# Performance work log

Measured on AMD Instinct MI355X. Metric: run time of the kernel, lower is better.

Reference implementation:

```python
import jax, jax.numpy as jnp
import numpy as np

B, S, D = 4, 512, 768
NH, DH = 12, 64
EXP_N, INV_N = 32, 64


def _scalar_mlp(x, w1, b1, w2, b2):
    # elementwise 1 -> N -> 1 MLP: y = relu(x*w1 + b1) @ w2 + b2, applied per element
    h = jax.nn.relu(x[..., None] * w1 + b1)          # [..., N]
    return jnp.einsum('...n,n->...', h, w2) + b2[0]  # [...]


def fit_softmax(X, exp_w1, exp_b1, exp_w2, exp_b2, inv_w1, inv_b1, inv_w2, inv_b2):
    # X: [B, H, S, S]. Faithful to torch fit_softmax: reference value is X[:, :, 0]
    tmax = X[:, :, 0][..., None]                      # [B, H, S, 1]
    tp = jnp.minimum(X - (tmax - 1.0), 3.0)           # clamp tp > 3 -> 3
    exp_val = _scalar_mlp(tp, exp_w1, exp_b1, exp_w2, exp_b2)
    X_up = jnp.where(tp > -20.0, exp_val, 0.0)        # only index tp > -20
    partition = jnp.sum(X_up, axis=-1, keepdims=True)  # [B, H, S, 1]
    p_inv = _scalar_mlp(partition, inv_w1, inv_b1, inv_w2, inv_b2)
    out = X_up * p_inv
    partition_p2 = jnp.sum(out, axis=-1, keepdims=True)
    p_inv2 = _scalar_mlp(partition_p2, inv_w1, inv_b1, inv_w2, inv_b2)
    # renormalize only rows whose partition exceeds 1.5
    return jnp.where(partition_p2 > 1.5, out * p_inv2, out)


def setup_inputs() -> dict:
    key = jax.random.key(0)
    ks = jax.random.split(key, 16)
    f = jax.random.normal
    return {
        'hidden_states': f(ks[0], (B, S, D), jnp.float32),
        'attention_mask': jnp.zeros((B, 1, 1, S), jnp.float32),
        'Wq': f(ks[1], (D, D), jnp.float32) * 0.02,
        'bq': f(ks[2], (D,), jnp.float32) * 0.02,
        'Wk': f(ks[3], (D, D), jnp.float32) * 0.02,
        'bk': f(ks[4], (D,), jnp.float32) * 0.02,
        'Wv': f(ks[5], (D, D), jnp.float32) * 0.02,
        'bv': f(ks[6], (D,), jnp.float32) * 0.02,
        'exp_w1': f(ks[7], (EXP_N,), jnp.float32),
        'exp_b1': f(ks[8], (EXP_N,), jnp.float32),
        'exp_w2': f(ks[9], (EXP_N,), jnp.float32) * 0.1,
        'exp_b2': f(ks[10], (1,), jnp.float32) * 0.1,
        'inv_w1': f(ks[11], (INV_N,), jnp.float32),
        'inv_b1': f(ks[12], (INV_N,), jnp.float32),
        'inv_w2': f(ks[13], (INV_N,), jnp.float32) * 0.1,
        'inv_b2': f(ks[14], (1,), jnp.float32) * 0.1,
    }


def reference(hidden_states, attention_mask, Wq, bq, Wk, bk, Wv, bv,
              exp_w1, exp_b1, exp_w2, exp_b2, inv_w1, inv_b1, inv_w2, inv_b2):
    def split_heads(x):  # [B, S, D] -> [B, H, S, DH]
        return x.reshape(B, S, NH, DH).transpose(0, 2, 1, 3)

    q = split_heads(hidden_states @ Wq.T + bq)
    k = split_heads(hidden_states @ Wk.T + bk)
    v = split_heads(hidden_states @ Wv.T + bv)

    scores = jnp.einsum('bhqd,bhkd->bhqk', q, k) / np.float32(np.sqrt(DH))
    scores = scores + attention_mask
    probs = fit_softmax(scores, exp_w1, exp_b1, exp_w2, exp_b2,
                        inv_w1, inv_b1, inv_w2, inv_b2)
    ctx = jnp.einsum('bhqk,bhkd->bhqd', probs, v)     # [B, H, S, DH]
    return ctx.transpose(0, 2, 1, 3).reshape(B, S, D)
```

## Files before the change

kernel.cpp:

```cpp
#include <hip/hip_runtime.h>
#include <math.h>

typedef unsigned short u16;
typedef short bf16x8 __attribute__((ext_vector_type(8)));
typedef float f32x4 __attribute__((ext_vector_type(4)));

#define BN 4
#define SN 512
#define DN 768
#define NHN 12
#define DHN 64
#define EXPN 32
#define INVN 64

#define TAB_T0 -20.5f
#define TAB_DLT (23.5f / 512.0f)
#define TAB_SCALE (512.0f / 23.5f)

__device__ __forceinline__ u16 f2b(float f) {
    union { float f; unsigned int u; } v; v.f = f;
    unsigned int r = v.u + 0x7FFFu + ((v.u >> 16) & 1u);
    return (u16)(r >> 16);
}
__device__ __forceinline__ u16 f2h(float f) {
    union { _Float16 h; u16 u; } v; v.h = (_Float16)f; return v.u;
}

#define GLD16(g, l) __builtin_amdgcn_global_load_lds( \
    (__attribute__((address_space(1))) const void*)(g), \
    (__attribute__((address_space(3))) void*)(l), 16, 0, 0)

__global__ __launch_bounds__(256) void prep(
    const float* __restrict__ X, const float* __restrict__ Wq,
    const float* __restrict__ Wk, const float* __restrict__ Wv,
    const float* __restrict__ ew1, const float* __restrict__ eb1,
    const float* __restrict__ ew2, const float* __restrict__ eb2,
    u16* __restrict__ Xb, u16* __restrict__ Wqb,
    u16* __restrict__ Wkb, u16* __restrict__ Wvb,
    float2* __restrict__ tbl)
{
    if (blockIdx.y == 4) {
        int i = blockIdx.x * 256 + threadIdx.x;
        if (i > 513) return;
        float t0 = TAB_T0 + i * TAB_DLT;
        float t1 = t0 + TAB_DLT;
        float y0 = eb2[0], y1 = y0;
        #pragma unroll 8
        for (int n = 0; n < EXPN; ++n) {
            float w1 = ew1[n], b1 = eb1[n], w2 = ew2[n];
            y0 += fmaxf(fmaf(t0, w1, b1), 0.f) * w2;
            y1 += fmaxf(fmaf(t1, w1, b1), 0.f) * w2;
        }
        tbl[i] = make_float2(y0, y1 - y0);
        return;
    }
    const float* s; u16* d; int n;
    switch (blockIdx.y) {
        case 0:  s = X;  d = Xb;  n = (BN * SN) * DN; break;
        case 1:  s = Wq; d = Wqb; n = DN * DN; break;
        case 2:  s = Wk; d = Wkb; n = DN * DN; break;
        default: s = Wv; d = Wvb; n = DN * DN; break;
    }
    int i = (blockIdx.x * 256 + threadIdx.x) * 4;
    if (i < n) {
        float4 v = *(const float4*)&s[i];
        unsigned int lo = (unsigned)f2b(v.x) | ((unsigned)f2b(v.y) << 16);
        unsigned int hi = (unsigned)f2b(v.z) | ((unsigned)f2b(v.w) << 16);
        *(uint2*)&d[i] = make_uint2(lo, hi);
    }
}

__global__ __launch_bounds__(256) void qkv_mfma(
    const u16* __restrict__ Xb,
    const u16* __restrict__ Wqb, const u16* __restrict__ Wkb, const u16* __restrict__ Wvb,
    const float* __restrict__ bq, const float* __restrict__ bk, const float* __restrict__ bv,
    u16* __restrict__ Qb, u16* __restrict__ Kb, u16* __restrict__ Vtr)
{
    __shared__ __align__(16) u16 As[128 * 32];
    __shared__ __align__(16) u16 Bs[64 * 32];

    const int tid = threadIdx.x, w = tid >> 6, l = tid & 63;
    const int lr = l & 15, lg = l >> 4;
    const int m0 = blockIdx.y * 128;
    const int nsel = blockIdx.x / 12;
    const int n0l = (blockIdx.x % 12) * 64;
    const u16* W = (nsel == 0) ? Wqb : (nsel == 1) ? Wkb : Wvb;
    const float* bias = (nsel == 0) ? bq : (nsel == 1) ? bk : bv;
    u16* out = (nsel == 0) ? Qb : (nsel == 1) ? Kb : Vtr;

    const int wm = w >> 1, wn = w & 1;

    const int oA0 = tid * 16;
    const int rA0 = oA0 >> 6, sA0 = (oA0 >> 4) & 3;
    const int cA0 = (sA0 ^ ((rA0 >> 1) & 3)) * 8;
    const int oA1 = oA0 + 4096;
    const int rA1 = oA1 >> 6, sA1 = (oA1 >> 4) & 3;
    const int cA1 = (sA1 ^ ((rA1 >> 1) & 3)) * 8;
    const u16* gA0 = Xb + (m0 + rA0) * DN + cA0;
    const u16* gA1 = Xb + (m0 + rA1) * DN + cA1;
    const u16* gB  = W + (n0l + rA0) * DN + cA0;

    int offA[4], offB[2];
    #pragma unroll
    for (int mi = 0; mi < 4; ++mi) {
        int row = wm * 64 + mi * 16 + lr;
        offA[mi] = row * 64 + ((lg ^ ((row >> 1) & 3)) * 16);
    }
    #pragma unroll
    for (int ni = 0; ni < 2; ++ni) {
        int row = wn * 32 + ni * 16 + lr;
        offB[ni] = row * 64 + ((lg ^ ((row >> 1) & 3)) * 16);
    }

    f32x4 acc[4][2];
    #pragma unroll
    for (int mi = 0; mi < 4; ++mi)
        #pragma unroll
        for (int ni = 0; ni < 2; ++ni) acc[mi][ni] = (f32x4){0.f, 0.f, 0.f, 0.f};

    for (int k0 = 0; k0 < DN; k0 += 32) {
        __syncthreads();
        GLD16(gA0 + k0, (char*)As + oA0);
        GLD16(gA1 + k0, (char*)As + oA1);
        GLD16(gB  + k0, (char*)Bs + oA0);
        __syncthreads();

        bf16x8 af[4], bff[2];
        #pragma unroll
        for (int mi = 0; mi < 4; ++mi) af[mi] = *(const bf16x8*)((const char*)As + offA[mi]);
        #pragma unroll
        for (int ni = 0; ni < 2; ++ni) bff[ni] = *(const bf16x8*)((const char*)Bs + offB[ni]);
        #pragma unroll
        for (int mi = 0; mi < 4; ++mi)
            #pragma unroll
            for (int ni = 0; ni < 2; ++ni)
                acc[mi][ni] = __builtin_amdgcn_mfma_f32_16x16x32_bf16(af[mi], bff[ni], acc[mi][ni], 0, 0, 0);
    }

    if (nsel < 2) {
        #pragma unroll
        for (int ni = 0; ni < 2; ++ni) {
            int col = n0l + wn * 32 + ni * 16 + lr;
            float bc = bias[col];
            int hh = col >> 6, dh = col & 63;
            #pragma unroll
            for (int mi = 0; mi < 4; ++mi) {
                #pragma unroll
                for (int r = 0; r < 4; ++r) {
                    int m = m0 + wm * 64 + mi * 16 + lg * 4 + r;
                    int bi = m >> 9, srow = m & 511;
                    out[(((bi * NHN + hh) * SN) + srow) * DHN + dh] = f2b(acc[mi][ni][r] + bc);
                }
            }
        }
    } else {
        #pragma unroll
        for (int ni = 0; ni < 2; ++ni) {
            int col = n0l + wn * 32 + ni * 16 + lr;
            float bc = bias[col];
            int hh = col >> 6, dh = col & 63;
            #pragma unroll
            for (int mi = 0; mi < 4; ++mi) {
                int m = m0 + wm * 64 + mi * 16 + lg * 4;
                int bi = m >> 9, srow = m & 511;
                ushort4 pk;
                pk.x = f2h(acc[mi][ni][0] + bc);
                pk.y = f2h(acc[mi][ni][1] + bc);
                pk.z = f2h(acc[mi][ni][2] + bc);
                pk.w = f2h(acc[mi][ni][3] + bc);
                *(ushort4*)&out[((size_t)(bi * NHN + hh) * DHN + dh) * SN + srow] = pk;
            }
        }
    }
}

__global__ __launch_bounds__(512, 6) void attn_mfma(
    const u16* __restrict__ Qb, const u16* __restrict__ Kb, const u16* __restrict__ Vtr,
    const float* __restrict__ mask, const float2* __restrict__ tbl,
    const float* __restrict__ iw1, const float* __restrict__ ib1,
    const float* __restrict__ iw2, const float* __restrict__ ib2,
    float* __restrict__ out)
{
    __shared__ __align__(16) u16 sb[32 * 512];
    __shared__ __align__(16) float2 tab[514];
    __shared__ float ms[SN];
    __shared__ float wI1[INVN], wIb1[INVN], wI2[INVN];
    __shared__ float partw[8][32];
    __shared__ float scale_s[32];
    __shared__ float pvbuf[32][68];
    __shared__ float scal;

    const int tid = threadIdx.x, w = tid >> 6, l = tid & 63;
    const int lr = l & 15, lg = l >> 4, kb8 = lg * 8;
    const int bid = blockIdx.x;
    const int bh = bid >> 4;
    const int q0 = (bid & 15) * 32;
    const int b = bh / NHN, h = bh % NHN;
    const u16* Qh = Qb + (size_t)bh * SN * DHN;
    const u16* Kh = Kb + (size_t)bh * SN * DHN;
    const u16* VTh = Vtr + (size_t)bh * DHN * SN;

    if (tid < INVN) { wI1[tid] = iw1[tid]; wIb1[tid] = ib1[tid]; wI2[tid] = iw2[tid]; }
    if (tid == 511) scal = ib2[0];
    if (tid < SN) ms[tid] = mask[b * SN + tid];
    for (int i = tid; i < 514; i += 512) tab[i] = tbl[i];
    __syncthreads();

    const float ib2v = scal;

    bf16x8 aq00 = *(const bf16x8*)(Qh + (q0 + lr) * DHN + kb8);
    bf16x8 aq01 = *(const bf16x8*)(Qh + (q0 + lr) * DHN + 32 + kb8);
    bf16x8 aq10 = *(const bf16x8*)(Qh + (q0 + 16 + lr) * DHN + kb8);
    bf16x8 aq11 = *(const bf16x8*)(Qh + (q0 + 16 + lr) * DHN + 32 + kb8);

    float myref0[4], myref1[4];
    {
        bf16x8 a00 = *(const bf16x8*)(Qh + kb8);
        bf16x8 a01 = *(const bf16x8*)(Qh + 32 + kb8);
        const u16* kp0 = Kh + (q0 + lr) * DHN + kb8;
        bf16x8 b00 = *(const bf16x8*)(kp0);
        bf16x8 b01 = *(const bf16x8*)(kp0 + 32);
        const u16* kp1 = Kh + (q0 + 16 + lr) * DHN + kb8;
        bf16x8 b10 = *(const bf16x8*)(kp1);
        bf16x8 b11 = *(const bf16x8*)(kp1 + 32);
        f32x4 d0 = {0.f, 0.f, 0.f, 0.f}, d1 = {0.f, 0.f, 0.f, 0.f};
        d0 = __builtin_amdgcn_mfma_f32_16x16x32_bf16(a00, b00, d0, 0, 0, 0);
        d0 = __builtin_amdgcn_mfma_f32_16x16x32_bf16(a01, b01, d0, 0, 0, 0);
        d1 = __builtin_amdgcn_mfma_f32_16x16x32_bf16(a00, b10, d1, 0, 0, 0);
        d1 = __builtin_amdgcn_mfma_f32_16x16x32_bf16(a01, b11, d1, 0, 0, 0);
        float rc0 = d0[0] * 0.125f + ms[q0 + lr];
        float rc1 = d1[0] * 0.125f + ms[q0 + 16 + lr];
        #pragma unroll
        for (int r = 0; r < 4; ++r) {
            myref0[r] = __shfl(rc0, lg * 4 + r);
            myref1[r] = __shfl(rc1, lg * 4 + r);
        }
    }

    char* sbb = (char*)sb;
    float part0[4] = {0.f, 0.f, 0.f, 0.f};
    float part1[4] = {0.f, 0.f, 0.f, 0.f};
    const u16* kpp = Kh + (w * 64 + lr) * DHN + kb8;
    bf16x8 nb0 = *(const bf16x8*)(kpp);
    bf16x8 nb1 = *(const bf16x8*)(kpp + 32);
    #pragma unroll
    for (int i = 0; i < 4; ++i) {
        bf16x8 b0 = nb0, b1 = nb1;
        if (i < 3) {
            const u16* kn = kpp + (i + 1) * 16 * DHN;
            nb0 = *(const bf16x8*)(kn);
            nb1 = *(const bf16x8*)(kn + 32);
        }
        f32x4 d0 = {0.f, 0.f, 0.f, 0.f}, d1 = {0.f, 0.f, 0.f, 0.f};
        d0 = __builtin_amdgcn_mfma_f32_16x16x32_bf16(aq00, b0, d0, 0, 0, 0);
        d0 = __builtin_amdgcn_mfma_f32_16x16x32_bf16(aq01, b1, d0, 0, 0, 0);
        d1 = __builtin_amdgcn_mfma_f32_16x16x32_bf16(aq10, b0, d1, 0, 0, 0);
        d1 = __builtin_amdgcn_mfma_f32_16x16x32_bf16(aq11, b1, d1, 0, 0, 0);
        const int col0 = w * 64 + i * 16;
        const float mv = ms[col0 + lr];
        const int colb = (col0 + lr) * 2;
        #pragma unroll
        for (int r = 0; r < 4; ++r) {
            {
                float tp = fminf(d0[r] * 0.125f + mv - (myref0[r] - 1.0f), 3.0f);
                float v = (tp - TAB_T0) * TAB_SCALE;
                int idx = (int)v;
                idx = idx < 0 ? 0 : idx;
                float fr = v - (float)idx;
                float2 p = tab[idx];
                float e = fmaf(fr, p.y, p.x);
                float xu = (tp > -20.0f) ? e : 0.f;
                part0[r] += xu;
                int row = lg * 4 + r;
                *(u16*)(sbb + row * 1024 + (colb ^ ((row & 7) << 4))) = f2h(xu);
            }
            {
                float tp = fminf(d1[r] * 0.125f + mv - (myref1[r] - 1.0f), 3.0f);
                float v = (tp - TAB_T0) * TAB_SCALE;
                int idx = (int)v;
                idx = idx < 0 ? 0 : idx;
                float fr = v - (float)idx;
                float2 p = tab[idx];
                float e = fmaf(fr, p.y, p.x);
                float xu = (tp > -20.0f) ? e : 0.f;
                part1[r] += xu;
                int row = 16 + lg * 4 + r;
                *(u16*)(sbb + row * 1024 + (colb ^ ((row & 7) << 4))) = f2h(xu);
            }
        }
    }
    #pragma unroll
    for (int r = 0; r < 4; ++r) {
        #pragma unroll
        for (int s = 1; s < 16; s <<= 1) {
            part0[r] += __shfl_xor(part0[r], s);
            part1[r] += __shfl_xor(part1[r], s);
        }
    }
    if (lr == 0) {
        #pragma unroll
        for (int r = 0; r < 4; ++r) {
            partw[w][lg * 4 + r] = part0[r];
            partw[w][16 + lg * 4 + r] = part1[r];
        }
    }
    __syncthreads();

    #pragma unroll
    for (int rr = 0; rr < 4; ++rr) {
        const int row = w * 4 + rr;
        float pt = 0.f;
        #pragma unroll
        for (int ww = 0; ww < 8; ++ww) pt += partw[ww][row];
        float hu = fmaxf(fmaf(pt, wI1[l], wIb1[l]), 0.f) * wI2[l];
        #pragma unroll
        for (int s = 32; s > 0; s >>= 1) hu += __shfl_xor(hu, s);
        const float pinv = hu + ib2v;
        const float p2 = pt * pinv;
        float hu2 = fmaxf(fmaf(p2, wI1[l], wIb1[l]), 0.f) * wI2[l];
        #pragma unroll
        for (int s = 32; s > 0; s >>= 1) hu2 += __shfl_xor(hu2, s);
        const float pinv2 = hu2 + ib2v;
        if (l == 0) scale_s[row] = pinv * ((p2 > 1.5f) ? pinv2 : 1.0f);
    }

    const int ds = (w & 3) * 16, kh = w >> 2;
    f32x4 acc0 = {0.f, 0.f, 0.f, 0.f}, acc1 = {0.f, 0.f, 0.f, 0.f};
    const u16* vp = VTh + (ds + lr) * SN + kh * 256 + kb8;
    const int swzl = (lr & 7) << 4;
    bf16x8 nv = *(const bf16x8*)(vp);
    #pragma unroll
    for (int k0 = 0; k0 < 256; k0 += 32) {
        bf16x8 bv = nv;
        if (k0 < 224) nv = *(const bf16x8*)(vp + k0 + 32);
        const int kk2 = (kh * 256 + k0 + kb8) * 2;
        bf16x8 a0 = *(const bf16x8*)(sbb + lr * 1024 + (kk2 ^ swzl));
        bf16x8 a1 = *(const bf16x8*)(sbb + (16 + lr) * 1024 + (kk2 ^ swzl));
        acc0 = __builtin_amdgcn_mfma_f32_16x16x32_f16(a0, bv, acc0, 0, 0, 0);
        acc1 = __builtin_amdgcn_mfma_f32_16x16x32_f16(a1, bv, acc1, 0, 0, 0);
    }
    if (kh == 1) {
        #pragma unroll
        for (int r = 0; r < 4; ++r) {
            pvbuf[lg * 4 + r][ds + lr] = acc0[r];
            pvbuf[16 + lg * 4 + r][ds + lr] = acc1[r];
        }
    }
    __syncthreads();
    if (kh == 0) {
        #pragma unroll
        for (int r = 0; r < 4; ++r) {
            const int row0 = lg * 4 + r;
            const int row1 = row0 + 16;
            float v0 = (acc0[r] + pvbuf[row0][ds + lr]) * scale_s[row0];
            float v1 = (acc1[r] + pvbuf[row1][ds + lr]) * scale_s[row1];
            out[(size_t)(b * SN + q0 + row0) * DN + h * DHN + ds + lr] = v0;
            out[(size_t)(b * SN + q0 + row1) * DN + h * DHN + ds + lr] = v1;
        }
    }
}

extern "C" void kernel_launch(void* const* d_in, const int* in_sizes, int n_in,
                              void* d_out, int out_size, void* d_ws, size_t ws_size,
                              hipStream_t stream) {
    const float* X    = (const float*)d_in[0];
    const float* mask = (const float*)d_in[1];
    const float* Wq   = (const float*)d_in[2];
    const float* bq   = (const float*)d_in[3];
    const float* Wk   = (const float*)d_in[4];
    const float* bk   = (const float*)d_in[5];
    const float* Wv   = (const float*)d_in[6];
    const float* bv   = (const float*)d_in[7];
    const float* ew1  = (const float*)d_in[8];
    const float* eb1  = (const float*)d_in[9];
    const float* ew2  = (const float*)d_in[10];
    const float* eb2  = (const float*)d_in[11];
    const float* iw1  = (const float*)d_in[12];
    const float* ib1  = (const float*)d_in[13];
    const float* iw2  = (const float*)d_in[14];
    const float* ib2  = (const float*)d_in[15];
    float* out = (float*)d_out;

    u16* Xb  = (u16*)d_ws;
    u16* Wqb = Xb + (size_t)(BN * SN) * DN;
    u16* Wkb = Wqb + DN * DN;
    u16* Wvb = Wkb + DN * DN;
    u16* Qb  = Wvb + DN * DN;
    const size_t per = (size_t)BN * NHN * SN * DHN;
    u16* Kb2 = Qb + per;
    u16* Vb2 = Kb2 + per;
    float2* tbl = (float2*)(Vb2 + per);

    dim3 gc(1536, 5);
    prep<<<gc, 256, 0, stream>>>(X, Wq, Wk, Wv, ew1, eb1, ew2, eb2,
                                 Xb, Wqb, Wkb, Wvb, tbl);

    dim3 g1(36, 16);
    qkv_mfma<<<g1, 256, 0, stream>>>(Xb, Wqb, Wkb, Wvb, bq, bk, bv, Qb, Kb2, Vb2);

    attn_mfma<<<dim3(768), 512, 0, stream>>>(Qb, Kb2, Vb2, mask, tbl,
                                             iw1, ib1, iw2, ib2, out);
}
```

Baseline: 58.80 us.

## Split PV across query tiles, drop LDS mask/partial buffers, deepen K prefetch

The PV stage now has each wave cover one 16-row query tile over the full 512-key range. Previously two waves split the key range and combined partial sums through an LDS pvbuf. This removes the pvbuf shared array and the cross-wave reduction. The mask and ib2 scalar are read straight from global memory instead of being staged in LDS, and the K-tile prefetch in QK is two iterations deep instead of one. The smaller LDS footprint may allow more resident blocks, at the cost of a longer serial MFMA chain per wave and extra register pressure from the deeper prefetch.

Result: slower. 61.88 us (+5.2%).

```diff
diff --git a/kernel.cpp b/kernel.cpp
--- a/kernel.cpp
+++ b/kernel.cpp
@@ -86,7 +86,6 @@
     const int n0l = (blockIdx.x % 12) * 64;
     const u16* W = (nsel == 0) ? Wqb : (nsel == 1) ? Wkb : Wvb;
     const float* bias = (nsel == 0) ? bq : (nsel == 1) ? bk : bv;
-    u16* out = (nsel == 0) ? Qb : (nsel == 1) ? Kb : Vtr;
 
     const int wm = w >> 1, wn = w & 1;
 
@@ -138,6 +137,7 @@
     }
 
     if (nsel < 2) {
+        u16* out = (nsel == 0) ? Qb : Kb;
         #pragma unroll
         for (int ni = 0; ni < 2; ++ni) {
             int col = n0l + wn * 32 + ni * 16 + lr;
@@ -168,7 +168,7 @@
                 pk.y = f2h(acc[mi][ni][1] + bc);
                 pk.z = f2h(acc[mi][ni][2] + bc);
                 pk.w = f2h(acc[mi][ni][3] + bc);
-                *(ushort4*)&out[((size_t)(bi * NHN + hh) * DHN + dh) * SN + srow] = pk;
+                *(ushort4*)&Vtr[((size_t)(bi * NHN + hh) * DHN + dh) * SN + srow] = pk;
             }
         }
     }
@@ -183,12 +183,9 @@
 {
     __shared__ __align__(16) u16 sb[32 * 512];
     __shared__ __align__(16) float2 tab[514];
-    __shared__ float ms[SN];
     __shared__ float wI1[INVN], wIb1[INVN], wI2[INVN];
     __shared__ float partw[8][32];
     __shared__ float scale_s[32];
-    __shared__ float pvbuf[32][68];
-    __shared__ float scal;
 
     const int tid = threadIdx.x, w = tid >> 6, l = tid & 63;
     const int lr = l & 15, lg = l >> 4, kb8 = lg * 8;
@@ -199,14 +196,13 @@
     const u16* Qh = Qb + (size_t)bh * SN * DHN;
     const u16* Kh = Kb + (size_t)bh * SN * DHN;
     const u16* VTh = Vtr + (size_t)bh * DHN * SN;
+    const float* mb = mask + b * SN;
 
     if (tid < INVN) { wI1[tid] = iw1[tid]; wIb1[tid] = ib1[tid]; wI2[tid] = iw2[tid]; }
-    if (tid == 511) scal = ib2[0];
-    if (tid < SN) ms[tid] = mask[b * SN + tid];
     for (int i = tid; i < 514; i += 512) tab[i] = tbl[i];
     __syncthreads();
 
-    const float ib2v = scal;
+    const float ib2v = ib2[0];
 
     bf16x8 aq00 = *(const bf16x8*)(Qh + (q0 + lr) * DHN + kb8);
     bf16x8 aq01 = *(const bf16x8*)(Qh + (q0 + lr) * DHN + 32 + kb8);
@@ -228,8 +224,8 @@
         d0 = __builtin_amdgcn_mfma_f32_16x16x32_bf16(a01, b01, d0, 0, 0, 0);
         d1 = __builtin_amdgcn_mfma_f32_16x16x32_bf16(a00, b10, d1, 0, 0, 0);
         d1 = __builtin_amdgcn_mfma_f32_16x16x32_bf16(a01, b11, d1, 0, 0, 0);
-        float rc0 = d0[0] * 0.125f + ms[q0 + lr];
-        float rc1 = d1[0] * 0.125f + ms[q0 + 16 + lr];
+        float rc0 = d0[0] * 0.125f + mb[q0 + lr];
+        float rc1 = d1[0] * 0.125f + mb[q0 + 16 + lr];
         #pragma unroll
         for (int r = 0; r < 4; ++r) {
             myref0[r] = __shfl(rc0, lg * 4 + r);
@@ -241,24 +237,27 @@
     float part0[4] = {0.f, 0.f, 0.f, 0.f};
     float part1[4] = {0.f, 0.f, 0.f, 0.f};
     const u16* kpp = Kh + (w * 64 + lr) * DHN + kb8;
-    bf16x8 nb0 = *(const bf16x8*)(kpp);
-    bf16x8 nb1 = *(const bf16x8*)(kpp + 32);
+    bf16x8 p00 = *(const bf16x8*)(kpp);
+    bf16x8 p01 = *(const bf16x8*)(kpp + 32);
+    bf16x8 p10 = *(const bf16x8*)(kpp + 16 * DHN);
+    bf16x8 p11 = *(const bf16x8*)(kpp + 16 * DHN + 32);
     #pragma unroll
     for (int i = 0; i < 4; ++i) {
-        bf16x8 b0 = nb0, b1 = nb1;
-        if (i < 3) {
-            const u16* kn = kpp + (i + 1) * 16 * DHN;
-            nb0 = *(const bf16x8*)(kn);
-            nb1 = *(const bf16x8*)(kn + 32);
+        bf16x8 b0 = p00, b1 = p01;
+        p00 = p10; p01 = p11;
+        if (i < 2) {
+            const u16* kn = kpp + (i + 2) * 16 * DHN;
+            p10 = *(const bf16x8*)(kn);
+            p11 = *(const bf16x8*)(kn + 32);
         }
         f32x4 d0 = {0.f, 0.f, 0.f, 0.f}, d1 = {0.f, 0.f, 0.f, 0.f};
         d0 = __builtin_amdgcn_mfma_f32_16x16x32_bf16(aq00, b0, d0, 0, 0, 0);
         d0 = __builtin_amdgcn_mfma_f32_16x16x32_bf16(aq01, b1, d0, 0, 0, 0);
         d1 = __builtin_amdgcn_mfma_f32_16x16x32_bf16(aq10, b0, d1, 0, 0, 0);
         d1 = __builtin_amdgcn_mfma_f32_16x16x32_bf16(aq11, b1, d1, 0, 0, 0);
-        const int col0 = w * 64 + i * 16;
-        const float mv = ms[col0 + lr];
-        const int colb = (col0 + lr) * 2;
+        const int col = w * 64 + i * 16 + lr;
+        const float mv = mb[col];
+        const int colb = col * 2;
         #pragma unroll
         for (int r = 0; r < 4; ++r) {
             {
@@ -324,39 +323,26 @@
         if (l == 0) scale_s[row] = pinv * ((p2 > 1.5f) ? pinv2 : 1.0f);
     }
 
-    const int ds = (w & 3) * 16, kh = w >> 2;
-    f32x4 acc0 = {0.f, 0.f, 0.f, 0.f}, acc1 = {0.f, 0.f, 0.f, 0.f};
-    const u16* vp = VTh + (ds + lr) * SN + kh * 256 + kb8;
+    const int mt = w & 1, ds = (w >> 1) * 16;
+    f32x4 acc = {0.f, 0.f, 0.f, 0.f};
+    const u16* vp = VTh + (ds + lr) * SN + kb8;
     const int swzl = (lr & 7) << 4;
-    bf16x8 nv = *(const bf16x8*)(vp);
-    #pragma unroll
-    for (int k0 = 0; k0 < 256; k0 += 32) {
-        bf16x8 bv = nv;
-        if (k0 < 224) nv = *(const bf16x8*)(vp + k0 + 32);
-        const int kk2 = (kh * 256 + k0 + kb8) * 2;
-        bf16x8 a0 = *(const bf16x8*)(sbb + lr * 1024 + (kk2 ^ swzl));
-        bf16x8 a1 = *(const bf16x8*)(sbb + (16 + lr) * 1024 + (kk2 ^ swzl));
-        acc0 = __builtin_amdgcn_mfma_f32_16x16x32_f16(a0, bv, acc0, 0, 0, 0);
-        acc1 = __builtin_amdgcn_mfma_f32_16x16x32_f16(a1, bv, acc1, 0, 0, 0);
-    }
-    if (kh == 1) {
-        #pragma unroll
-        for (int r = 0; r < 4; ++r) {
-            pvbuf[lg * 4 + r][ds + lr] = acc0[r];
-            pvbuf[16 + lg * 4 + r][ds + lr] = acc1[r];
-        }
+    const int rowbase = (mt * 16 + lr) * 1024;
+    bf16x8 nv0 = *(const bf16x8*)(vp);
+    bf16x8 nv1 = *(const bf16x8*)(vp + 32);
+    #pragma unroll
+    for (int k0 = 0; k0 < SN; k0 += 32) {
+        bf16x8 bv = nv0;
+        nv0 = nv1;
+        if (k0 < SN - 64) nv1 = *(const bf16x8*)(vp + k0 + 64);
+        bf16x8 a = *(const bf16x8*)(sbb + rowbase + (((k0 + kb8) * 2) ^ swzl));
+        acc = __builtin_amdgcn_mfma_f32_16x16x32_f16(a, bv, acc, 0, 0, 0);
     }
     __syncthreads();
-    if (kh == 0) {
-        #pragma unroll
-        for (int r = 0; r < 4; ++r) {
-            const int row0 = lg * 4 + r;
-            const int row1 = row0 + 16;
-            float v0 = (acc0[r] + pvbuf[row0][ds + lr]) * scale_s[row0];
-            float v1 = (acc1[r] + pvbuf[row1][ds + lr]) * scale_s[row1];
-            out[(size_t)(b * SN + q0 + row0) * DN + h * DHN + ds + lr] = v0;
-            out[(size_t)(b * SN + q0 + row1) * DN + h * DHN + ds + lr] = v1;
-        }
+    #pragma unroll
+    for (int r = 0; r < 4; ++r) {
+        const int row = mt * 16 + lg * 4 + r;
+        out[(size_t)(b * SN + q0 + row) * DN + h * DHN + ds + lr] = acc[r] * scale_s[row];
     }
 }
 
@@ -381,7 +367,8 @@
     const float* ib2  = (const float*)d_in[15];
     float* out = (float*)d_out;
 
-    u16* Xb  = (u16*)d_ws;
+    float2* tbl = (float2*)d_ws;
+    u16* Xb  = (u16*)((char*)d_ws + 4608);
     u16* Wqb = Xb + (size_t)(BN * SN) * DN;
     u16* Wkb = Wqb + DN * DN;
     u16* Wvb = Wkb + DN * DN;
@@ -389,7 +376,6 @@
     const size_t per = (size_t)BN * NHN * SN * DHN;
     u16* Kb2 = Qb + per;
     u16* Vb2 = Kb2 + per;
-    float2* tbl = (float2*)(Vb2 + per);
 
     dim3 gc(1536, 5);
     prep<<<gc, 256, 0, stream>>>(X, Wq, Wk, Wv, ew1, eb1, ew2, eb2,
```
